# Kernel tuning notes

Hardware: AMD Instinct MI355X
Metric: run time of the kernel (lower is better)

The kernel has to match this reference:

```python
import jax, jax.numpy as jnp
import numpy as np

B, S, D = 4, 2048, 1024
NEG_BIG = -1.0e9


def setup_inputs() -> dict:
    key = jax.random.key(0)
    ks = jax.random.split(key, 9)
    scale = 1.0 / np.sqrt(D)
    inp = {
        "v": jax.random.normal(ks[0], (B, S, D), dtype=jnp.float32),
        "k": jax.random.normal(ks[1], (B, S, D), dtype=jnp.float32),
        "q": jax.random.normal(ks[2], (B, S, D), dtype=jnp.float32),
        # causal mask: 1 where attention is disallowed (j > i), broadcast over batch
        "mask": jnp.triu(jnp.ones((1, S, S), dtype=jnp.float32), k=1),
        "Wq": jax.random.normal(ks[3], (D, D), dtype=jnp.float32) * scale,
        "bq": jnp.zeros((D,), dtype=jnp.float32),
        "Wk": jax.random.normal(ks[4], (D, D), dtype=jnp.float32) * scale,
        "bk": jnp.zeros((D,), dtype=jnp.float32),
        "Wv": jax.random.normal(ks[5], (D, D), dtype=jnp.float32) * scale,
        "bv": jnp.zeros((D,), dtype=jnp.float32),
    }
    return inp


def reference(v, k, q, mask, Wq, bq, Wk, bk, Wv, bv):
    # Dense projections (Keras Dense: x @ W + b)
    qp = q @ Wq + bq  # [B, S, D]
    kp = k @ Wk + bk  # [B, S, D]
    vp = v @ Wv + bv  # [B, S, D]

    dk = jnp.asarray(D, dtype=qp.dtype)
    logits = jnp.einsum("bqd,bkd->bqk", qp, kp) / jnp.sqrt(dk)  # [B, S, S]
    logits = logits + mask * NEG_BIG
    attn = jax.nn.softmax(logits, axis=-1)  # [B, S, S]
    out = jnp.einsum("bqk,bkd->bqd", attn, vp)  # [B, S, D]
    return out, attn
```

## Files before the change

kernel.cpp:

```cpp
#include <hip/hip_runtime.h>
#include <hip/hip_bf16.h>
#include <cstdint>

#define BATCH 4
#define S_LEN 2048
#define D_DIM 1024

typedef __attribute__((ext_vector_type(4))) float f32x4_t;
typedef __attribute__((ext_vector_type(8))) __bf16 bf16x8_t;

__device__ __forceinline__ ushort f32_to_bf16(float f) {
    uint32_t u = __float_as_uint(f);
    uint32_t r = (u + 0x7FFFu + ((u >> 16) & 1u)) >> 16;
    return (ushort)r;
}

__global__ __launch_bounds__(256)
void cvt3_kernel(const float* __restrict__ a, const float* __restrict__ b,
                 const float* __restrict__ c, ushort* __restrict__ out, int n4) {
    int z = blockIdx.y;
    const float* src = (z == 0) ? a : ((z == 1) ? b : c);
    ushort* dst = out + (size_t)z * n4 * 4;
    int idx = blockIdx.x * blockDim.x + threadIdx.x;
    int stride = gridDim.x * blockDim.x;
    const float4* in4 = (const float4*)src;
    ushort4* out4 = (ushort4*)dst;
    for (int i = idx; i < n4; i += stride) {
        float4 v = in4[i];
        ushort4 o;
        o.x = f32_to_bf16(v.x);
        o.y = f32_to_bf16(v.y);
        o.z = f32_to_bf16(v.z);
        o.w = f32_to_bf16(v.w);
        out4[i] = o;
    }
}

__global__ __launch_bounds__(256)
void transpose_cvt_kernel(const float* __restrict__ in, ushort* __restrict__ out,
                          int rows, int cols) {
    __shared__ ushort tile[64][66];
    int r0 = blockIdx.y * 64, c0 = blockIdx.x * 64;
    int t = threadIdx.x;
    int cr = t & 63;
    int cc = t >> 6;
    #pragma unroll
    for (int i = 0; i < 16; ++i) {
        int r = cc * 16 + i;
        tile[r][cr] = f32_to_bf16(in[(size_t)(r0 + r) * cols + (c0 + cr)]);
    }
    __syncthreads();
    #pragma unroll
    for (int i = 0; i < 16; ++i) {
        int c = cc * 16 + i;
        out[(size_t)(c0 + c) * rows + (r0 + cr)] = tile[cr][c];
    }
}

__global__ __launch_bounds__(256)
void bias_concat_kernel(const float* __restrict__ bq, const float* __restrict__ bk,
                        const float* __restrict__ bv, float* __restrict__ out) {
    int i = blockIdx.x * blockDim.x + threadIdx.x;
    if (i < D_DIM) out[i] = bq[i];
    else if (i < 2 * D_DIM) out[i] = bk[i - D_DIM];
    else if (i < 3 * D_DIM) out[i] = bv[i - 2 * D_DIM];
}

enum { MODE_PROJ = 0, MODE_LOGITS = 1, MODE_OUT = 2 };

#define PRE_BAR() do { __builtin_amdgcn_s_barrier(); \
    asm volatile("s_waitcnt lgkmcnt(0)" ::: "memory"); \
    __builtin_amdgcn_sched_barrier(0); } while (0)
#define POST_BAR() do { __builtin_amdgcn_sched_barrier(0); \
    __builtin_amdgcn_s_barrier(); } while (0)
#define GATE(N) do { asm volatile("s_waitcnt vmcnt(" #N ")" ::: "memory"); \
    __builtin_amdgcn_sched_barrier(0); } while (0)

#define GLOAD(dst, src) __builtin_amdgcn_global_load_lds( \
    (const __attribute__((address_space(1))) uint32_t*)(src), \
    (__attribute__((address_space(3))) uint32_t*)(dst), 16, 0, 0)

__device__ __forceinline__ void xcd_swizzle(int& bc, int& br) {
    int gx = gridDim.x;
    int nwg = gx * gridDim.y;
    int orig = blockIdx.y * gx + blockIdx.x;
    int xcd = orig & 7, idx = orig >> 3;
    int wgid = xcd * (nwg >> 3) + idx;
    bc = wgid % gx;
    br = wgid / gx;
}

template<int MODE>
__global__ __launch_bounds__(512, 2)
void gemm_q_kernel(const ushort* __restrict__ A, const ushort* __restrict__ Bt,
                   const float* __restrict__ bias, void* __restrict__ Cout,
                   ushort* __restrict__ vpT,
                   int K, int lda, int ldb, int ldc,
                   long strideA, long strideC, float scale) {
    __shared__ ushort As[2][256 * 64];
    __shared__ ushort Bs[2][256 * 64];
    int bc, br;
    xcd_swizzle(bc, br);
    int bz = blockIdx.z;
    if (MODE == MODE_LOGITS && bc > br) return;
    const ushort* Ab = (MODE == MODE_PROJ) ? A + (size_t)(bc >> 2) * strideA
                                           : A + (size_t)bz * strideA;
    const ushort* Bb = (MODE == MODE_PROJ) ? Bt : Bt + (size_t)bz * strideA;
    int brow = br * 256, bcol = bc * 256;
    int t = threadIdx.x, lane = t & 63, wid = t >> 6;
    int wr = wid >> 2, wc = wid & 3;
    int nkt = K / 64;

    const ushort* aSrc[4];
    const ushort* bSrc[4];
    int oL[4];
    #pragma unroll
    for (int j = 0; j < 4; ++j) {
        int o = (j * 512 + t) * 16;
        int row = o >> 7;
        int colb = (o & 127) ^ ((row & 7) << 4);
        oL[j] = o >> 1;
        aSrc[j] = Ab + (size_t)(brow + row) * lda + (colb >> 1);
        bSrc[j] = Bb + (size_t)(bcol + row) * ldb + (colb >> 1);
    }
    auto stgA = [&](int tk, int slot, int j0, int j1) {
        ushort* d = &As[slot][0];
        GLOAD(d + oL[j0], aSrc[j0] + tk * 64);
        GLOAD(d + oL[j1], aSrc[j1] + tk * 64);
    };
    auto stgB = [&](int tk, int slot, int j0, int j1) {
        ushort* d = &Bs[slot][0];
        GLOAD(d + oL[j0], bSrc[j0] + tk * 64);
        GLOAD(d + oL[j1], bSrc[j1] + tk * 64);
    };

    int rdA[2][4], rdB[4];
    #pragma unroll
    for (int mh = 0; mh < 2; ++mh)
        #pragma unroll
        for (int m = 0; m < 4; ++m) {
            int ra = wr * 128 + mh * 64 + m * 16 + (lane & 15);
            int cb = (lane >> 4) * 16;
            rdA[mh][m] = ra * 128 + (cb ^ ((ra & 7) << 4));
        }
    #pragma unroll
    for (int nf = 0; nf < 4; ++nf) {
        int rb = (nf >> 1) * 128 + wc * 32 + (nf & 1) * 16 + (lane & 15);
        int cb = (lane >> 4) * 16;
        rdB[nf] = rb * 128 + (cb ^ ((rb & 7) << 4));
    }

    f32x4_t acc[8][4];
    #pragma unroll
    for (int m = 0; m < 8; ++m)
        #pragma unroll
        for (int n = 0; n < 4; ++n)
            acc[m][n] = (f32x4_t){0.f, 0.f, 0.f, 0.f};

    bf16x8_t af[4][2], bfr[4][2];

    auto readAh = [&](int slot, int mh) {
        const char* base = (const char*)&As[slot][0];
        #pragma unroll
        for (int m = 0; m < 4; ++m) {
            af[m][0] = *(const bf16x8_t*)(base + rdA[mh][m]);
            af[m][1] = *(const bf16x8_t*)(base + (rdA[mh][m] ^ 64));
        }
    };
    auto readBh = [&](int slot, int nh) {
        const char* base = (const char*)&Bs[slot][0];
        #pragma unroll
        for (int n = 0; n < 2; ++n) {
            int nf = nh * 2 + n;
            bfr[nf][0] = *(const bf16x8_t*)(base + rdB[nf]);
            bfr[nf][1] = *(const bf16x8_t*)(base + (rdB[nf] ^ 64));
        }
    };

#define QUAD(MH, NH)                                                                \
    do { __builtin_amdgcn_s_setprio(1);                                             \
        _Pragma("unroll") for (int m = 0; m < 4; ++m)                               \
        _Pragma("unroll") for (int n = 0; n < 2; ++n)                               \
        _Pragma("unroll") for (int ks = 0; ks < 2; ++ks)                            \
            acc[(MH) * 4 + m][(NH) * 2 + n] = __builtin_amdgcn_mfma_f32_16x16x32_bf16( \
                af[m][ks], bfr[(NH) * 2 + n][ks], acc[(MH) * 4 + m][(NH) * 2 + n], 0, 0, 0); \
        __builtin_amdgcn_s_setprio(0); } while (0)

    stgB(0, 0, 0, 1); stgA(0, 0, 0, 2); stgB(0, 0, 2, 3); stgA(0, 0, 1, 3);
    GATE(4);
    __builtin_amdgcn_s_barrier();

    for (int y = 0; y < nkt; ++y) {
        int cur = y & 1, nxt = cur ^ 1;
        bool st = (y + 1 < nkt);
        readAh(cur, 0); readBh(cur, 0);
        if (st) stgB(y + 1, nxt, 0, 1);
        PRE_BAR(); QUAD(0, 0);
        if (st) { GATE(4); } else { GATE(2); }
        POST_BAR();
        readBh(cur, 1);
        if (st) stgA(y + 1, nxt, 0, 2);
        PRE_BAR(); QUAD(0, 1);
        if (st) { GATE(4); } else { GATE(0); }
        POST_BAR();
        readAh(cur, 1);
        if (st) stgB(y + 1, nxt, 2, 3);
        PRE_BAR(); QUAD(1, 1); POST_BAR();
        if (st) stgA(y + 1, nxt, 1, 3);
        PRE_BAR(); QUAD(1, 0);
        if (st) { GATE(4); }
        POST_BAR();
    }
#undef QUAD

    int crow0 = brow + wr * 128 + ((lane >> 4) * 4);
    int ccol0 = wc * 32 + (lane & 15);
    if (MODE == MODE_PROJ) {
        #pragma unroll
        for (int mf = 0; mf < 8; ++mf) {
            int rowg = crow0 + (mf >> 2) * 64 + (mf & 3) * 16;
            #pragma unroll
            for (int nf = 0; nf < 4; ++nf) {
                int gcol = bcol + (nf >> 1) * 128 + ccol0 + (nf & 1) * 16;
                float bv = bias[gcol];
                if (bc < 8) {
                    ushort* C = (ushort*)Cout;
                    #pragma unroll
                    for (int j = 0; j < 4; ++j)
                        C[(size_t)(rowg + j) * 2048 + gcol] = f32_to_bf16(acc[mf][nf][j] + bv);
                } else {
                    int d = gcol - 2048;
                    int b = rowg >> 11, s = rowg & 2047;
                    ushort4 o;
                    o.x = f32_to_bf16(acc[mf][nf][0] + bv);
                    o.y = f32_to_bf16(acc[mf][nf][1] + bv);
                    o.z = f32_to_bf16(acc[mf][nf][2] + bv);
                    o.w = f32_to_bf16(acc[mf][nf][3] + bv);
                    *(ushort4*)&vpT[(size_t)b * D_DIM * S_LEN + (size_t)d * S_LEN + s] = o;
                }
            }
        }
    } else {
        float* C = (float*)Cout + (size_t)bz * strideC;
        #pragma unroll
        for (int mf = 0; mf < 8; ++mf) {
            int rowg = crow0 + (mf >> 2) * 64 + (mf & 3) * 16;
            #pragma unroll
            for (int nf = 0; nf < 4; ++nf) {
                int col = bcol + (nf >> 1) * 128 + ccol0 + (nf & 1) * 16;
                #pragma unroll
                for (int j = 0; j < 4; ++j)
                    C[(size_t)(rowg + j) * ldc + col] = acc[mf][nf][j] * scale;
            }
        }
    }
}

#define LGKM(N) do { asm volatile("s_waitcnt lgkmcnt(" #N ")" ::: "memory"); \
    __builtin_amdgcn_sched_barrier(0); } while (0)

__global__ __launch_bounds__(512, 2)
void gemm_out_kernel(const ushort* __restrict__ A, const ushort* __restrict__ Bt,
                     void* __restrict__ Cout,
                     int K, int lda, int ldb, int ldc,
                     long strideA, long strideB, long strideC, float scale) {
    __shared__ ushort As[3][256 * 64];
    __shared__ ushort Bs[3][128 * 64];
    int bc, br;
    xcd_swizzle(bc, br);
    int bz = blockIdx.z;
    const ushort* Ab = A + (size_t)bz * strideA;
    const ushort* Bb = Bt + (size_t)bz * strideB;
    int brow = br * 256, bcol = bc * 128;
    int t = threadIdx.x, lane = t & 63, wid = t >> 6;
    int wr = wid >> 1, wc = wid & 1;
    int nkt = min(K / 64, (brow + 256) / 64);

    const ushort* aSrc[4];
    const ushort* bSrc[2];
    int oA[4], oB[2];
    #pragma unroll
    for (int j = 0; j < 4; ++j) {
        int o = (j * 512 + t) * 16;
        int row = o >> 7;
        int col = (o & 127) ^ ((row & 7) << 4);
        oA[j] = o >> 1;
        aSrc[j] = Ab + (size_t)(brow + row) * lda + (col >> 1);
    }
    #pragma unroll
    for (int j = 0; j < 2; ++j) {
        int o = (j * 512 + t) * 16;
        int row = o >> 7;
        int col = (o & 127) ^ ((row & 7) << 4);
        oB[j] = o >> 1;
        bSrc[j] = Bb + (size_t)(bcol + row) * ldb + (col >> 1);
    }
    auto stage = [&](int tk, int slot) {
        ushort* dA = &As[slot][0];
        ushort* dB = &Bs[slot][0];
        #pragma unroll
        for (int j = 0; j < 4; ++j) GLOAD(dA + oA[j], aSrc[j] + tk * 64);
        #pragma unroll
        for (int j = 0; j < 2; ++j) GLOAD(dB + oB[j], bSrc[j] + tk * 64);
    };

    int rdA[4][2], rdB[4][2];
    #pragma unroll
    for (int m = 0; m < 4; ++m) {
        int ra = wr * 64 + m * 16 + (lane & 15);
        #pragma unroll
        for (int ks = 0; ks < 2; ++ks) {
            int cb = ks * 64 + ((lane >> 4) * 16);
            rdA[m][ks] = ra * 128 + (cb ^ ((ra & 7) << 4));
        }
    }
    #pragma unroll
    for (int n = 0; n < 4; ++n) {
        int rb = wc * 64 + n * 16 + (lane & 15);
        #pragma unroll
        for (int ks = 0; ks < 2; ++ks) {
            int cb = ks * 64 + ((lane >> 4) * 16);
            rdB[n][ks] = rb * 128 + (cb ^ ((rb & 7) << 4));
        }
    }

    f32x4_t acc[4][4];
    #pragma unroll
    for (int m = 0; m < 4; ++m)
        #pragma unroll
        for (int n = 0; n < 4; ++n)
            acc[m][n] = (f32x4_t){0.f, 0.f, 0.f, 0.f};

    bf16x8_t aE0[4], aE1[4], bE0[4], bE1[4];
    bf16x8_t aO0[4], aO1[4], bO0[4], bO1[4];

#define MF16(AV, BV)                                                           \
    do { __builtin_amdgcn_s_setprio(1);                                        \
        _Pragma("unroll") for (int m = 0; m < 4; ++m)                          \
        _Pragma("unroll") for (int n = 0; n < 4; ++n)                          \
            acc[m][n] = __builtin_amdgcn_mfma_f32_16x16x32_bf16(               \
                AV[m], BV[n], acc[m][n], 0, 0, 0);                             \
        __builtin_amdgcn_s_setprio(0); } while (0)

#define TILE_BODY(X, CA0, CA1, CB0, CB1, NA0, NA1, NB0, NB1)                   \
    do {                                                                       \
        int x_ = (X);                                                          \
        __builtin_amdgcn_s_barrier();                                          \
        if (x_ + 2 < nkt) stage(x_ + 2, (x_ + 2) % 3);                         \
        if (x_ + 1 < nkt) { if (x_ + 2 < nkt) { GATE(6); } else { GATE(0); } } \
        __builtin_amdgcn_s_barrier();                                          \
        {                                                                      \
            const char* nA = (const char*)&As[(x_ + 1) % 3][0];                \
            const char* nB = (const char*)&Bs[(x_ + 1) % 3][0];                \
            if (x_ + 1 < nkt) {                                                \
                _Pragma("unroll") for (int n = 0; n < 4; ++n)                  \
                    NB0[n] = *(const bf16x8_t*)(nB + rdB[n][0]);               \
                _Pragma("unroll") for (int m = 0; m < 4; ++m)                  \
                    NA0[m] = *(const bf16x8_t*)(nA + rdA[m][0]);               \
                LGKM(8);                                                       \
            } else { LGKM(0); }                                                \
            MF16(CA0, CB0);                                                    \
            if (x_ + 1 < nkt) {                                                \
                _Pragma("unroll") for (int n = 0; n < 4; ++n)                  \
                    NB1[n] = *(const bf16x8_t*)(nB + rdB[n][1]);               \
                _Pragma("unroll") for (int m = 0; m < 4; ++m)                  \
                    NA1[m] = *(const bf16x8_t*)(nA + rdA[m][1]);               \
            }                                                                  \
            MF16(CA1, CB1);                                                    \
        }                                                                      \
    } while (0)

    stage(0, 0);
    stage(1, 1);
    GATE(6);
    __builtin_amdgcn_s_barrier();
    {
        const char* pA = (const char*)&As[0][0];
        const char* pB = (const char*)&Bs[0][0];
        #pragma unroll
        for (int n = 0; n < 4; ++n) bE0[n] = *(const bf16x8_t*)(pB + rdB[n][0]);
        #pragma unroll
        for (int m = 0; m < 4; ++m) aE0[m] = *(const bf16x8_t*)(pA + rdA[m][0]);
        #pragma unroll
        for (int n = 0; n < 4; ++n) bE1[n] = *(const bf16x8_t*)(pB + rdB[n][1]);
        #pragma unroll
        for (int m = 0; m < 4; ++m) aE1[m] = *(const bf16x8_t*)(pA + rdA[m][1]);
    }

    int nhalf = nkt >> 1;
    for (int it = 0; it < nhalf; ++it) {
        int x = 2 * it;
        TILE_BODY(x,     aE0, aE1, bE0, bE1, aO0, aO1, bO0, bO1);
        TILE_BODY(x + 1, aO0, aO1, bO0, bO1, aE0, aE1, bE0, bE1);
    }
#undef TILE_BODY
#undef MF16

    float* C = (float*)Cout + (size_t)bz * strideC;
    int crow0 = brow + wr * 64 + ((lane >> 4) * 4);
    int ccol0 = bcol + wc * 64 + (lane & 15);
    #pragma unroll
    for (int mf = 0; mf < 4; ++mf)
        #pragma unroll
        for (int nf = 0; nf < 4; ++nf) {
            int col = ccol0 + nf * 16;
            #pragma unroll
            for (int j = 0; j < 4; ++j) {
                int rowg = crow0 + mf * 16 + j;
                C[(size_t)rowg * ldc + col] = acc[mf][nf][j] * scale;
            }
        }
}

__global__ __launch_bounds__(256)
void softmax_causal_kernel(float* __restrict__ attn, ushort* __restrict__ attn_bf) {
    int rowid = blockIdx.x;
    int i = rowid & (S_LEN - 1);
    float* lrow = attn + (size_t)rowid * S_LEN;
    ushort* brw = attn_bf + (size_t)rowid * S_LEN;
    int t = threadIdx.x;
    int nvalid = i + 1;
    int nact = (nvalid + 255) >> 8;

    float vals[8];
    float lmax = -1e30f;
    #pragma unroll
    for (int it = 0; it < 8; ++it) {
        if (it < nact) {
            int j = it * 256 + t;
            float v = (j < nvalid) ? lrow[j] : -1e30f;
            vals[it] = v;
            lmax = fmaxf(lmax, v);
        }
    }
    #pragma unroll
    for (int off = 32; off > 0; off >>= 1)
        lmax = fmaxf(lmax, __shfl_xor(lmax, off));

    __shared__ float redm[4];
    __shared__ float reds[4];
    int wave = t >> 6, lane = t & 63;
    if (lane == 0) redm[wave] = lmax;
    __syncthreads();
    float m = fmaxf(fmaxf(redm[0], redm[1]), fmaxf(redm[2], redm[3]));

    float lsum = 0.f;
    #pragma unroll
    for (int it = 0; it < 8; ++it) {
        if (it < nact) {
            int j = it * 256 + t;
            float e = (j < nvalid) ? __expf(vals[it] - m) : 0.f;
            vals[it] = e;
            lsum += e;
        }
    }
    #pragma unroll
    for (int off = 32; off > 0; off >>= 1)
        lsum += __shfl_xor(lsum, off);
    if (lane == 0) reds[wave] = lsum;
    __syncthreads();
    float denom = reds[0] + reds[1] + reds[2] + reds[3];
    float inv = 1.f / denom;

    #pragma unroll
    for (int it = 0; it < 8; ++it) {
        int j = it * 256 + t;
        if (it < nact) {
            float p = vals[it] * inv;
            lrow[j] = p;
            brw[j] = f32_to_bf16(p);
        } else {
            lrow[j] = 0.f;
            brw[j] = 0;
        }
    }
}

extern "C" void kernel_launch(void* const* d_in, const int* in_sizes, int n_in,
                              void* d_out, int out_size, void* d_ws, size_t ws_size,
                              hipStream_t stream) {
    const float* v  = (const float*)d_in[0];
    const float* k  = (const float*)d_in[1];
    const float* q  = (const float*)d_in[2];
    const float* Wq = (const float*)d_in[4];
    const float* bq = (const float*)d_in[5];
    const float* Wk = (const float*)d_in[6];
    const float* bk = (const float*)d_in[7];
    const float* Wv = (const float*)d_in[8];
    const float* bv = (const float*)d_in[9];

    float* out  = (float*)d_out;
    float* attn = (float*)d_out + (size_t)BATCH * S_LEN * D_DIM;

    char* ws = (char*)d_ws;
    const size_t NTOK = (size_t)BATCH * S_LEN;
    ushort* xqkv  = (ushort*)(ws);
    ushort* qkvp  = (ushort*)(ws + 48u * 1024 * 1024);
    ushort* vpT   = (ushort*)(ws + 80u * 1024 * 1024);
    ushort* WT    = (ushort*)(ws + 96u * 1024 * 1024);
    float*  bias3 = (float*)(ws + 102u * 1024 * 1024);
    ushort* attn_bf = (ushort*)(ws);

    const int n4 = (int)(NTOK * D_DIM / 4);
    cvt3_kernel<<<dim3(1024, 3), dim3(256), 0, stream>>>(q, k, v, xqkv, n4);

    transpose_cvt_kernel<<<dim3(16, 16), dim3(256), 0, stream>>>(Wq, WT, D_DIM, D_DIM);
    transpose_cvt_kernel<<<dim3(16, 16), dim3(256), 0, stream>>>(Wk, WT + (size_t)D_DIM * D_DIM, D_DIM, D_DIM);
    transpose_cvt_kernel<<<dim3(16, 16), dim3(256), 0, stream>>>(Wv, WT + 2 * (size_t)D_DIM * D_DIM, D_DIM, D_DIM);
    bias_concat_kernel<<<dim3(12), dim3(256), 0, stream>>>(bq, bk, bv, bias3);

    gemm_q_kernel<MODE_PROJ><<<dim3(12, 32, 1), dim3(512), 0, stream>>>(
        xqkv, WT, bias3, qkvp, vpT, D_DIM, D_DIM, D_DIM, 2048,
        (long)NTOK * D_DIM, 0, 1.f);

    gemm_q_kernel<MODE_LOGITS><<<dim3(8, 8, BATCH), dim3(512), 0, stream>>>(
        qkvp, qkvp + D_DIM, nullptr, attn, nullptr, D_DIM, 2048, 2048, S_LEN,
        (long)S_LEN * 2048, (long)S_LEN * S_LEN, 0.03125f);

    softmax_causal_kernel<<<dim3((int)NTOK), dim3(256), 0, stream>>>(attn, attn_bf);

    gemm_out_kernel<<<dim3(8, 8, BATCH), dim3(512), 0, stream>>>(
        attn_bf, vpT, out, S_LEN, S_LEN, S_LEN, D_DIM,
        (long)S_LEN * S_LEN, (long)D_DIM * S_LEN, (long)S_LEN * D_DIM, 1.f);
}
```

Before: 220.0 us.

## Fold Wk into Wq product to skip K projection GEMM

Logits are rewritten as q·(Wq Wkᵀ)·kᵀ. A small GEMM forms M = Wq·Wkᵀ, the projection GEMM then computes q·M together with the V projection, and the logits GEMM reads raw bf16 k directly, so the separate K projection is removed. Bias terms are folded into a per-key vector w = k·(Wk·bq) that is added in softmax. bk is dropped because it only adds a per-query constant that softmax cancels. The trade-offs are an extra bf16 rounding of the fused weight matrix and the bias handling, which changes numerics, plus several small extra kernels. The bf16 zeroing of the masked part of attn_bf in softmax is also removed.

```diff
diff --git a/kernel.cpp b/kernel.cpp
--- a/kernel.cpp
+++ b/kernel.cpp
@@ -16,23 +16,52 @@
 }
 
 __global__ __launch_bounds__(256)
-void cvt3_kernel(const float* __restrict__ a, const float* __restrict__ b,
-                 const float* __restrict__ c, ushort* __restrict__ out, int n4) {
+void cvt_all_kernel(const float* __restrict__ q, const float* __restrict__ k,
+                    const float* __restrict__ v, const float* __restrict__ wk,
+                    const float* __restrict__ wq,
+                    ushort* __restrict__ xqkv, ushort* __restrict__ xw, int n4) {
     int z = blockIdx.y;
-    const float* src = (z == 0) ? a : ((z == 1) ? b : c);
-    ushort* dst = out + (size_t)z * n4 * 4;
+    const float* src;
+    ushort* dst;
+    int n;
+    if (z < 3) {
+        src = (z == 0) ? q : ((z == 1) ? k : v);
+        dst = xqkv + (size_t)z * n4 * 4;
+        n = n4;
+    } else {
+        src = nullptr; dst = nullptr; n = 0;
+    }
     int idx = blockIdx.x * blockDim.x + threadIdx.x;
     int stride = gridDim.x * blockDim.x;
-    const float4* in4 = (const float4*)src;
-    ushort4* out4 = (ushort4*)dst;
-    for (int i = idx; i < n4; i += stride) {
-        float4 v = in4[i];
-        ushort4 o;
-        o.x = f32_to_bf16(v.x);
-        o.y = f32_to_bf16(v.y);
-        o.z = f32_to_bf16(v.z);
-        o.w = f32_to_bf16(v.w);
-        out4[i] = o;
+    if (z < 3) {
+        const float4* in4 = (const float4*)src;
+        ushort4* out4 = (ushort4*)dst;
+        for (int i = idx; i < n; i += stride) {
+            float4 vv = in4[i];
+            ushort4 o;
+            o.x = f32_to_bf16(vv.x);
+            o.y = f32_to_bf16(vv.y);
+            o.z = f32_to_bf16(vv.z);
+            o.w = f32_to_bf16(vv.w);
+            out4[i] = o;
+        }
+    } else {
+        int nw = D_DIM * D_DIM / 4;
+        const float4* ik = (const float4*)wk;
+        const float4* iq = (const float4*)wq;
+        ushort4* ok = (ushort4*)xw;
+        ushort4* oq = (ushort4*)(xw + (size_t)D_DIM * D_DIM);
+        for (int i = idx; i < nw; i += stride) {
+            float4 a = ik[i];
+            ushort4 o;
+            o.x = f32_to_bf16(a.x); o.y = f32_to_bf16(a.y);
+            o.z = f32_to_bf16(a.z); o.w = f32_to_bf16(a.w);
+            ok[i] = o;
+            float4 b = iq[i];
+            o.x = f32_to_bf16(b.x); o.y = f32_to_bf16(b.y);
+            o.z = f32_to_bf16(b.z); o.w = f32_to_bf16(b.w);
+            oq[i] = o;
+        }
     }
 }
 
@@ -58,15 +87,47 @@
 }
 
 __global__ __launch_bounds__(256)
-void bias_concat_kernel(const float* __restrict__ bq, const float* __restrict__ bk,
-                        const float* __restrict__ bv, float* __restrict__ out) {
+void fill_kernel(const float* __restrict__ bv, float* __restrict__ bias2) {
     int i = blockIdx.x * blockDim.x + threadIdx.x;
-    if (i < D_DIM) out[i] = bq[i];
-    else if (i < 2 * D_DIM) out[i] = bk[i - D_DIM];
-    else if (i < 3 * D_DIM) out[i] = bv[i - 2 * D_DIM];
-}
-
-enum { MODE_PROJ = 0, MODE_LOGITS = 1, MODE_OUT = 2 };
+    bias2[i] = (i < D_DIM) ? 0.f : bv[i - D_DIM];
+}
+
+__global__ __launch_bounds__(256)
+void hv_kernel(const float* __restrict__ Wk, const float* __restrict__ bq,
+               float* __restrict__ hv) {
+    int wave = threadIdx.x >> 6, lane = threadIdx.x & 63;
+    int r = blockIdx.x * 4 + wave;
+    const float* row = Wk + (size_t)r * D_DIM;
+    float s = 0.f;
+    #pragma unroll
+    for (int it = 0; it < 16; ++it)
+        s += row[it * 64 + lane] * bq[it * 64 + lane];
+    #pragma unroll
+    for (int off = 32; off > 0; off >>= 1)
+        s += __shfl_xor(s, off);
+    if (lane == 0) hv[r] = s;
+}
+
+__global__ __launch_bounds__(256)
+void wvec_kernel(const ushort* __restrict__ xk, const float* __restrict__ hv,
+                 float* __restrict__ w) {
+    int wave = threadIdx.x >> 6, lane = threadIdx.x & 63;
+    int r = blockIdx.x * 4 + wave;
+    const ushort* row = xk + (size_t)r * D_DIM + lane * 16;
+    const float* hp = hv + lane * 16;
+    float s = 0.f;
+    #pragma unroll
+    for (int it = 0; it < 16; ++it) {
+        uint32_t u = row[it];
+        s += __uint_as_float(u << 16) * hp[it];
+    }
+    #pragma unroll
+    for (int off = 32; off > 0; off >>= 1)
+        s += __shfl_xor(s, off);
+    if (lane == 0) w[r] = s * 0.03125f;
+}
+
+enum { MODE_PROJ = 0, MODE_MT = 1, MODE_LOGITS = 2 };
 
 #define PRE_BAR() do { __builtin_amdgcn_s_barrier(); \
     asm volatile("s_waitcnt lgkmcnt(0)" ::: "memory"); \
@@ -94,7 +155,7 @@
 __global__ __launch_bounds__(512, 2)
 void gemm_q_kernel(const ushort* __restrict__ A, const ushort* __restrict__ Bt,
                    const float* __restrict__ bias, void* __restrict__ Cout,
-                   ushort* __restrict__ vpT,
+                   ushort* __restrict__ vpTp,
                    int K, int lda, int ldb, int ldc,
                    long strideA, long strideC, float scale) {
     __shared__ ushort As[2][256 * 64];
@@ -105,7 +166,7 @@
     if (MODE == MODE_LOGITS && bc > br) return;
     const ushort* Ab = (MODE == MODE_PROJ) ? A + (size_t)(bc >> 2) * strideA
                                            : A + (size_t)bz * strideA;
-    const ushort* Bb = (MODE == MODE_PROJ) ? Bt : Bt + (size_t)bz * strideA;
+    const ushort* Bb = (MODE == MODE_LOGITS) ? Bt + (size_t)bz * strideA : Bt;
     int brow = br * 256, bcol = bc * 256;
     int t = threadIdx.x, lane = t & 63, wid = t >> 6;
     int wr = wid >> 2, wc = wid & 3;
@@ -223,21 +284,34 @@
             for (int nf = 0; nf < 4; ++nf) {
                 int gcol = bcol + (nf >> 1) * 128 + ccol0 + (nf & 1) * 16;
                 float bv = bias[gcol];
-                if (bc < 8) {
+                if (gcol < D_DIM) {
                     ushort* C = (ushort*)Cout;
                     #pragma unroll
                     for (int j = 0; j < 4; ++j)
-                        C[(size_t)(rowg + j) * 2048 + gcol] = f32_to_bf16(acc[mf][nf][j] + bv);
+                        C[(size_t)(rowg + j) * D_DIM + gcol] = f32_to_bf16(acc[mf][nf][j] + bv);
                 } else {
-                    int d = gcol - 2048;
+                    int d = gcol - D_DIM;
                     int b = rowg >> 11, s = rowg & 2047;
                     ushort4 o;
                     o.x = f32_to_bf16(acc[mf][nf][0] + bv);
                     o.y = f32_to_bf16(acc[mf][nf][1] + bv);
                     o.z = f32_to_bf16(acc[mf][nf][2] + bv);
                     o.w = f32_to_bf16(acc[mf][nf][3] + bv);
-                    *(ushort4*)&vpT[(size_t)b * D_DIM * S_LEN + (size_t)d * S_LEN + s] = o;
+                    *(ushort4*)&vpTp[((size_t)b * D_DIM + d) * S_LEN + s] = o;
                 }
+            }
+        }
+    } else if (MODE == MODE_MT) {
+        ushort* C = (ushort*)Cout;
+        #pragma unroll
+        for (int mf = 0; mf < 8; ++mf) {
+            int rowg = crow0 + (mf >> 2) * 64 + (mf & 3) * 16;
+            #pragma unroll
+            for (int nf = 0; nf < 4; ++nf) {
+                int gcol = bcol + (nf >> 1) * 128 + ccol0 + (nf & 1) * 16;
+                #pragma unroll
+                for (int j = 0; j < 4; ++j)
+                    C[(size_t)(rowg + j) * ldc + gcol] = f32_to_bf16(acc[mf][nf][j]);
             }
         }
     } else {
@@ -413,11 +487,13 @@
 }
 
 __global__ __launch_bounds__(256)
-void softmax_causal_kernel(float* __restrict__ attn, ushort* __restrict__ attn_bf) {
+void softmax_causal_kernel(float* __restrict__ attn, ushort* __restrict__ attn_bf,
+                           const float* __restrict__ w) {
     int rowid = blockIdx.x;
     int i = rowid & (S_LEN - 1);
     float* lrow = attn + (size_t)rowid * S_LEN;
     ushort* brw = attn_bf + (size_t)rowid * S_LEN;
+    const float* wv = w + (rowid & ~(S_LEN - 1));
     int t = threadIdx.x;
     int nvalid = i + 1;
     int nact = (nvalid + 255) >> 8;
@@ -428,7 +504,7 @@
     for (int it = 0; it < 8; ++it) {
         if (it < nact) {
             int j = it * 256 + t;
-            float v = (j < nvalid) ? lrow[j] : -1e30f;
+            float v = (j < nvalid) ? (lrow[j] + wv[j]) : -1e30f;
             vals[it] = v;
             lmax = fmaxf(lmax, v);
         }
@@ -471,7 +547,6 @@
             brw[j] = f32_to_bf16(p);
         } else {
             lrow[j] = 0.f;
-            brw[j] = 0;
         }
     }
 }
@@ -485,7 +560,6 @@
     const float* Wq = (const float*)d_in[4];
     const float* bq = (const float*)d_in[5];
     const float* Wk = (const float*)d_in[6];
-    const float* bk = (const float*)d_in[7];
     const float* Wv = (const float*)d_in[8];
     const float* bv = (const float*)d_in[9];
 
@@ -493,31 +567,41 @@
     float* attn = (float*)d_out + (size_t)BATCH * S_LEN * D_DIM;
 
     char* ws = (char*)d_ws;
+    const size_t MB = 1024u * 1024u;
     const size_t NTOK = (size_t)BATCH * S_LEN;
     ushort* xqkv  = (ushort*)(ws);
-    ushort* qkvp  = (ushort*)(ws + 48u * 1024 * 1024);
-    ushort* vpT   = (ushort*)(ws + 80u * 1024 * 1024);
-    ushort* WT    = (ushort*)(ws + 96u * 1024 * 1024);
-    float*  bias3 = (float*)(ws + 102u * 1024 * 1024);
+    ushort* xq    = xqkv;
+    ushort* xk    = xqkv + NTOK * D_DIM;
+    ushort* qq    = (ushort*)(ws + 48 * MB);
+    ushort* vpT   = (ushort*)(ws + 64 * MB);
+    ushort* Bcat  = (ushort*)(ws + 80 * MB);
+    ushort* xW    = (ushort*)(ws + 84 * MB);
+    float*  bias2 = (float*)(ws + 88 * MB);
+    float*  hvb   = (float*)(ws + 88 * MB + 8192);
+    float*  wvec  = (float*)(ws + 88 * MB + 16384);
     ushort* attn_bf = (ushort*)(ws);
 
     const int n4 = (int)(NTOK * D_DIM / 4);
-    cvt3_kernel<<<dim3(1024, 3), dim3(256), 0, stream>>>(q, k, v, xqkv, n4);
-
-    transpose_cvt_kernel<<<dim3(16, 16), dim3(256), 0, stream>>>(Wq, WT, D_DIM, D_DIM);
-    transpose_cvt_kernel<<<dim3(16, 16), dim3(256), 0, stream>>>(Wk, WT + (size_t)D_DIM * D_DIM, D_DIM, D_DIM);
-    transpose_cvt_kernel<<<dim3(16, 16), dim3(256), 0, stream>>>(Wv, WT + 2 * (size_t)D_DIM * D_DIM, D_DIM, D_DIM);
-    bias_concat_kernel<<<dim3(12), dim3(256), 0, stream>>>(bq, bk, bv, bias3);
-
-    gemm_q_kernel<MODE_PROJ><<<dim3(12, 32, 1), dim3(512), 0, stream>>>(
-        xqkv, WT, bias3, qkvp, vpT, D_DIM, D_DIM, D_DIM, 2048,
-        (long)NTOK * D_DIM, 0, 1.f);
+    cvt_all_kernel<<<dim3(1024, 4), dim3(256), 0, stream>>>(q, k, v, Wk, Wq, xqkv, xW, n4);
+    transpose_cvt_kernel<<<dim3(16, 16), dim3(256), 0, stream>>>(Wv, Bcat + (size_t)D_DIM * D_DIM, D_DIM, D_DIM);
+    fill_kernel<<<dim3(8), dim3(256), 0, stream>>>(bv, bias2);
+    hv_kernel<<<dim3(256), dim3(256), 0, stream>>>(Wk, bq, hvb);
+    wvec_kernel<<<dim3(2048), dim3(256), 0, stream>>>(xk, hvb, wvec);
+
+    gemm_q_kernel<MODE_MT><<<dim3(4, 4, 1), dim3(512), 0, stream>>>(
+        xW, xW + (size_t)D_DIM * D_DIM, nullptr, Bcat, nullptr,
+        D_DIM, D_DIM, D_DIM, D_DIM, 0, 0, 1.f);
+
+    gemm_q_kernel<MODE_PROJ><<<dim3(8, 32, 1), dim3(512), 0, stream>>>(
+        xqkv, Bcat, bias2, qq, vpT,
+        D_DIM, D_DIM, D_DIM, 2048, (long)2 * NTOK * D_DIM, 0, 1.f);
 
     gemm_q_kernel<MODE_LOGITS><<<dim3(8, 8, BATCH), dim3(512), 0, stream>>>(
-        qkvp, qkvp + D_DIM, nullptr, attn, nullptr, D_DIM, 2048, 2048, S_LEN,
-        (long)S_LEN * 2048, (long)S_LEN * S_LEN, 0.03125f);
-
-    softmax_causal_kernel<<<dim3((int)NTOK), dim3(256), 0, stream>>>(attn, attn_bf);
+        qq, xk, nullptr, attn, nullptr,
+        D_DIM, D_DIM, D_DIM, S_LEN,
+        (long)S_LEN * D_DIM, (long)S_LEN * S_LEN, 0.03125f);
+
+    softmax_causal_kernel<<<dim3((int)NTOK), dim3(256), 0, stream>>>(attn, attn_bf, wvec);
 
     gemm_out_kernel<<<dim3(8, 8, BATCH), dim3(512), 0, stream>>>(
         attn_bf, vpT, out, S_LEN, S_LEN, S_LEN, D_DIM,
```

Result: no change. 219.6 us (-0.2%).
